# Performance work log

Hardware: AMD Instinct MI355X
Metric: run time of the kernel (lower is better)

The kernel has to match this reference:

```python
import jax, jax.numpy as jnp
import numpy as np

B, IN, P, H, OUT = 131072, 40, 128, 256, 1

def setup_inputs() -> dict:
    key = jax.random.key(0)
    ks = jax.random.split(key, 10)
    s_in, s_h = 1.0 / np.sqrt(IN), 1.0 / np.sqrt(H)
    return {
        "x_step": jax.random.normal(ks[0], (B, 1, IN), jnp.float32),
        "hidden_in": jax.random.normal(ks[1], (1, B, H), jnp.float32),
        "W_proj": jax.random.uniform(ks[2], (P, IN), jnp.float32, -s_in, s_in),
        "b_proj": jax.random.uniform(ks[3], (P,), jnp.float32, -s_in, s_in),
        "W_ih": jax.random.uniform(ks[4], (3 * H, P), jnp.float32, -s_h, s_h),
        "W_hh": jax.random.uniform(ks[5], (3 * H, H), jnp.float32, -s_h, s_h),
        "b_ih": jax.random.uniform(ks[6], (3 * H,), jnp.float32, -s_h, s_h),
        "b_hh": jax.random.uniform(ks[7], (3 * H,), jnp.float32, -s_h, s_h),
        "W_head": jax.random.uniform(ks[8], (OUT, H), jnp.float32, -s_h, s_h),
        "b_head": jax.random.uniform(ks[9], (OUT,), jnp.float32, -s_h, s_h),
    }

def reference(x_step, hidden_in, W_proj, b_proj, W_ih, W_hh, b_ih, b_hh, W_head, b_head):
    # input projection: [B,1,IN] -> [B,P]
    x = jnp.einsum('bi,pi->bp', x_step[:, 0, :], W_proj) + b_proj
    h = hidden_in[0]  # [B,H]
    # single GRU step (PyTorch gate layout: reset, update, new)
    gi = jnp.einsum('bp,gp->bg', x, W_ih) + b_ih  # [B,3H]
    gh = jnp.einsum('bh,gh->bg', h, W_hh) + b_hh  # [B,3H]
    i_r, i_z, i_n = jnp.split(gi, 3, axis=-1)
    h_r, h_z, h_n = jnp.split(gh, 3, axis=-1)
    r = jax.nn.sigmoid(i_r + h_r)
    z = jax.nn.sigmoid(i_z + h_z)
    n = jnp.tanh(i_n + r * h_n)
    h_new = (1.0 - z) * n + z * h  # [B,H]
    pred = jnp.einsum('bh,oh->bo', h_new, W_head) + b_head  # [B,OUT]
    return pred[:, None, :], h_new[None]  # ([B,1,OUT], [1,B,H])
```

## Files before the change

kernel.cpp:

```cpp
#include <hip/hip_runtime.h>

#define B_N 131072
#define IN_N 40
#define H_N 256

typedef __bf16 bf16x8 __attribute__((ext_vector_type(8)));
typedef __bf16 bf16x4 __attribute__((ext_vector_type(4)));
typedef float f32x4 __attribute__((ext_vector_type(4)));

#define MFMA(a, b, c) __builtin_amdgcn_mfma_f32_16x16x32_bf16(a, b, c, 0, 0, 0)

#define WSF 0
#define WSH 49152
#define WSBI 245760
#define PREP_N (245760 + 768 + B_N)

__global__ void prep(const float* __restrict__ Wp, const float* __restrict__ bp,
                     const float* __restrict__ Wih, const float* __restrict__ Whh,
                     const float* __restrict__ bih, const float* __restrict__ bhead,
                     __bf16* __restrict__ wsb, float* __restrict__ out) {
  int i = blockIdx.x * 256 + threadIdx.x;
  if (i < WSH) {
    int g = i >> 6, kk = i & 63;
    float v = 0.f;
    if (kk < IN_N) {
      for (int p = 0; p < 128; ++p) v += Wih[g * 128 + p] * Wp[p * IN_N + kk];
    }
    wsb[i] = (__bf16)v;
  } else if (i < WSBI) {
    wsb[i] = (__bf16)Whh[i - WSH];
  } else if (i < WSBI + 768) {
    int g = i - WSBI;
    float v = bih[g];
    for (int p = 0; p < 128; ++p) v += Wih[g * 128 + p] * bp[p];
    ((float*)(wsb + WSBI))[g] = v;
  } else if (i < PREP_N) {
    out[i - (WSBI + 768)] = bhead[0];
  }
}

__global__ __launch_bounds__(512, 2) void gru_v6(
    const float* __restrict__ x, const float* __restrict__ h0,
    const __bf16* __restrict__ wsb, const float* __restrict__ bhh,
    const float* __restrict__ Whead, float* __restrict__ out) {
  __shared__ __bf16 hs[2][64][264];
  __shared__ __bf16 xs[2][64][72];

  const int tid = threadIdx.x;
  const int lane = tid & 63;
  const int w = tid >> 6;
  const int l15 = lane & 15;
  const int l4 = lane >> 4;
  const int koff = l4 * 8;

  const int b = blockIdx.x;
  const int v = (b & 7) * 64 + (b >> 3);
  const int half = v & 1;
  const int tile0 = (v >> 1) * 8;
  const int col = half * 128 + w * 16 + l15;

  const __bf16* WH = wsb + WSH;
  const __bf16* WF = wsb + WSF;
  bf16x8 whR[8], whZ[8], whN[8], wfR[2], wfZ[2], wfN[2];
#pragma unroll
  for (int ks = 0; ks < 8; ++ks) {
    const int k = ks * 32 + koff;
    whR[ks] = *reinterpret_cast<const bf16x8*>(WH + (size_t)col * 256 + k);
    whZ[ks] = *reinterpret_cast<const bf16x8*>(WH + (size_t)(256 + col) * 256 + k);
    whN[ks] = *reinterpret_cast<const bf16x8*>(WH + (size_t)(512 + col) * 256 + k);
  }
#pragma unroll
  for (int ks = 0; ks < 2; ++ks) {
    const int k = ks * 32 + koff;
    wfR[ks] = *reinterpret_cast<const bf16x8*>(WF + (size_t)col * 64 + k);
    wfZ[ks] = *reinterpret_cast<const bf16x8*>(WF + (size_t)(256 + col) * 64 + k);
    wfN[ks] = *reinterpret_cast<const bf16x8*>(WF + (size_t)(512 + col) * 64 + k);
  }
  const float* bfused = (const float*)(wsb + WSBI);
  const float bR = bfused[col] + bhh[col];
  const float bZ = bfused[256 + col] + bhh[256 + col];
  const float bI = bfused[512 + col];
  const float bH = bhh[512 + col];
  const float whead = Whead[col];

  auto stage = [&](int buf, int row0) {
    const float* hb = h0 + (size_t)row0 * H_N;
#pragma unroll
    for (int j = 0; j < 8; ++j) {
      const int flat = (tid + j * 512) * 4;
      const int r = flat >> 8, c = flat & 255;
      float4 vv = *reinterpret_cast<const float4*>(hb + flat);
      bf16x4 u;
      u[0] = (__bf16)vv.x; u[1] = (__bf16)vv.y; u[2] = (__bf16)vv.z; u[3] = (__bf16)vv.w;
      *reinterpret_cast<bf16x4*>(&hs[buf][r][c]) = u;
    }
    const float* xb = x + (size_t)row0 * IN_N;
#pragma unroll
    for (int j = 0; j < 5; ++j) {
      const int i = tid + j * 512;
      xs[buf][i / 40][i % 40] = (__bf16)xb[i];
    }
#pragma unroll
    for (int j = 0; j < 3; ++j) {
      const int i = tid + j * 512;
      xs[buf][i / 24][40 + i % 24] = (__bf16)0.f;
    }
  };

  stage(0, tile0 * 64);
  __syncthreads();

  for (int t = 0; t < 8; ++t) {
    const int cur = t & 1;
    const int row0 = (tile0 + t) * 64;
    if (t < 7) stage(cur ^ 1, row0 + 64);

    f32x4 aR[4], aZ[4], aI[4], aH[4];
#pragma unroll
    for (int mi = 0; mi < 4; ++mi) {
      aR[mi] = (f32x4){bR, bR, bR, bR};
      aZ[mi] = (f32x4){bZ, bZ, bZ, bZ};
      aI[mi] = (f32x4){bI, bI, bI, bI};
      aH[mi] = (f32x4){bH, bH, bH, bH};
    }
#pragma unroll
    for (int ks = 0; ks < 2; ++ks) {
#pragma unroll
      for (int mi = 0; mi < 4; ++mi) {
        const bf16x8 a = *reinterpret_cast<const bf16x8*>(&xs[cur][mi * 16 + l15][ks * 32 + koff]);
        aR[mi] = MFMA(a, wfR[ks], aR[mi]);
        aZ[mi] = MFMA(a, wfZ[ks], aZ[mi]);
        aI[mi] = MFMA(a, wfN[ks], aI[mi]);
      }
    }
#pragma unroll
    for (int ks = 0; ks < 8; ++ks) {
#pragma unroll
      for (int mi = 0; mi < 4; ++mi) {
        const bf16x8 a = *reinterpret_cast<const bf16x8*>(&hs[cur][mi * 16 + l15][ks * 32 + koff]);
        aR[mi] = MFMA(a, whR[ks], aR[mi]);
        aZ[mi] = MFMA(a, whZ[ks], aZ[mi]);
        aH[mi] = MFMA(a, whN[ks], aH[mi]);
      }
    }
    float ps[4][4];
#pragma unroll
    for (int mi = 0; mi < 4; ++mi) {
#pragma unroll
      for (int r = 0; r < 4; ++r) {
        const int row = mi * 16 + l4 * 4 + r;
        const float rg = 1.f / (1.f + __expf(-aR[mi][r]));
        const float zg = 1.f / (1.f + __expf(-aZ[mi][r]));
        const float e2 = __expf(2.f * (aI[mi][r] + rg * aH[mi][r]));
        const float ng = (e2 - 1.f) / (e2 + 1.f);
        const float hv = (float)hs[cur][row][col];
        const float hn = (1.f - zg) * ng + zg * hv;
        out[(size_t)B_N + (size_t)(row0 + row) * H_N + col] = hn;
        ps[mi][r] = hn * whead;
      }
    }
#pragma unroll
    for (int mi = 0; mi < 4; ++mi)
#pragma unroll
      for (int r = 0; r < 4; ++r) {
        float s = ps[mi][r];
        s += __shfl_xor(s, 1);
        s += __shfl_xor(s, 2);
        s += __shfl_xor(s, 4);
        s += __shfl_xor(s, 8);
        if (l15 == 0) atomicAdd(&out[row0 + mi * 16 + l4 * 4 + r], s);
      }
    __syncthreads();
  }
}

extern "C" void kernel_launch(void* const* d_in, const int* in_sizes, int n_in,
                              void* d_out, int out_size, void* d_ws, size_t ws_size,
                              hipStream_t stream) {
  const float* x     = (const float*)d_in[0];
  const float* h0    = (const float*)d_in[1];
  const float* Wp    = (const float*)d_in[2];
  const float* bp    = (const float*)d_in[3];
  const float* Wih   = (const float*)d_in[4];
  const float* Whh   = (const float*)d_in[5];
  const float* bih   = (const float*)d_in[6];
  const float* bhh   = (const float*)d_in[7];
  const float* Whead = (const float*)d_in[8];
  const float* bhead = (const float*)d_in[9];
  float* out = (float*)d_out;
  __bf16* wsb = (__bf16*)d_ws;

  prep<<<(PREP_N + 255) / 256, 256, 0, stream>>>(Wp, bp, Wih, Whh, bih, bhead, wsb, out);
  gru_v6<<<512, 512, 0, stream>>>(x, h0, wsb, bhh, Whead, out);
}
```

Measured before the change: 216.2 us.

## Stream weight K-slices through LDS with async global_load_lds and larger row tiles

Weights are no longer held in registers per wave. They are pre-permuted in prep into K-slice-major tiles and streamed into double-buffered LDS via global_load_lds, one slice per step with a barrier each. Each block now computes a 128-row by 128-column tile, with waves arranged 2x4, and register-staged h/x prefetch for the next tile. This frees registers and raises per-wave MFMA work, but adds 10 barriers per tile, drops occupancy to one block per CU, and re-reads h0 in fp32 from global memory for the update.

Measured after the change: 421.9 us. 95.2% more time.

```diff
diff --git a/kernel.cpp b/kernel.cpp
--- a/kernel.cpp
+++ b/kernel.cpp
@@ -6,12 +6,13 @@
 
 typedef __bf16 bf16x8 __attribute__((ext_vector_type(8)));
 typedef __bf16 bf16x4 __attribute__((ext_vector_type(4)));
+typedef __bf16 bf16x2 __attribute__((ext_vector_type(2)));
 typedef float f32x4 __attribute__((ext_vector_type(4)));
 
 #define MFMA(a, b, c) __builtin_amdgcn_mfma_f32_16x16x32_bf16(a, b, c, 0, 0, 0)
 
-#define WSF 0
-#define WSH 49152
+#define WSGH 0
+#define WSGI 196608
 #define WSBI 245760
 #define PREP_N (245760 + 768 + B_N)
 
@@ -20,15 +21,21 @@
                      const float* __restrict__ bih, const float* __restrict__ bhead,
                      __bf16* __restrict__ wsb, float* __restrict__ out) {
   int i = blockIdx.x * 256 + threadIdx.x;
-  if (i < WSH) {
-    int g = i >> 6, kk = i & 63;
+  if (i < WSGI) {
+    int e8 = i & 7, col = (i >> 3) & 127, q = (i >> 10) & 3,
+        hf = (i >> 12) & 1, ks = (i >> 13) & 7, g = i >> 16;
+    int gcol = hf * 128 + col, k = ks * 32 + q * 8 + e8;
+    wsb[i] = (__bf16)Whh[(g * 256 + gcol) * 256 + k];
+  } else if (i < WSBI) {
+    int j = i - WSGI;
+    int e8 = j & 7, col = (j >> 3) & 127, q = (j >> 10) & 3,
+        hf = (j >> 12) & 1, ks2 = (j >> 13) & 1, g = j >> 14;
+    int gcol = hf * 128 + col, k = ks2 * 32 + q * 8 + e8;
     float v = 0.f;
-    if (kk < IN_N) {
-      for (int p = 0; p < 128; ++p) v += Wih[g * 128 + p] * Wp[p * IN_N + kk];
-    }
+    if (k < IN_N)
+      for (int p = 0; p < 128; ++p)
+        v += Wih[(g * 256 + gcol) * 128 + p] * Wp[p * IN_N + k];
     wsb[i] = (__bf16)v;
-  } else if (i < WSBI) {
-    wsb[i] = (__bf16)Whh[i - WSH];
   } else if (i < WSBI + 768) {
     int g = i - WSBI;
     float v = bih[g];
@@ -39,12 +46,19 @@
   }
 }
 
-__global__ __launch_bounds__(512, 2) void gru_v6(
+__device__ __forceinline__ void gload16(const __bf16* g, __bf16* l) {
+  __builtin_amdgcn_global_load_lds(
+      (const __attribute__((address_space(1))) void*)g,
+      (__attribute__((address_space(3))) void*)l, 16, 0, 0);
+}
+
+__global__ __launch_bounds__(512, 1) void gru_v11(
     const float* __restrict__ x, const float* __restrict__ h0,
     const __bf16* __restrict__ wsb, const float* __restrict__ bhh,
     const float* __restrict__ Whead, float* __restrict__ out) {
-  __shared__ __bf16 hs[2][64][264];
-  __shared__ __bf16 xs[2][64][72];
+  __shared__ __bf16 hs[128][264];
+  __shared__ __bf16 xs[128][72];
+  __shared__ __bf16 Bb[2][12288];
 
   const int tid = threadIdx.x;
   const int lane = tid & 63;
@@ -52,124 +66,162 @@
   const int l15 = lane & 15;
   const int l4 = lane >> 4;
   const int koff = l4 * 8;
-
-  const int b = blockIdx.x;
-  const int v = (b & 7) * 64 + (b >> 3);
-  const int half = v & 1;
-  const int tile0 = (v >> 1) * 8;
-  const int col = half * 128 + w * 16 + l15;
-
-  const __bf16* WH = wsb + WSH;
-  const __bf16* WF = wsb + WSF;
-  bf16x8 whR[8], whZ[8], whN[8], wfR[2], wfZ[2], wfN[2];
-#pragma unroll
-  for (int ks = 0; ks < 8; ++ks) {
-    const int k = ks * 32 + koff;
-    whR[ks] = *reinterpret_cast<const bf16x8*>(WH + (size_t)col * 256 + k);
-    whZ[ks] = *reinterpret_cast<const bf16x8*>(WH + (size_t)(256 + col) * 256 + k);
-    whN[ks] = *reinterpret_cast<const bf16x8*>(WH + (size_t)(512 + col) * 256 + k);
+  const int rw = w >> 2, cw = w & 3;
+
+  const int hf = blockIdx.x >> 8;
+  const int rgrp = blockIdx.x & 255;
+  const size_t row0 = (size_t)rgrp * 512;
+
+  const int colL = cw * 32 + l15;
+  const int col0 = hf * 128 + colL;
+  const int bofs = l4 * 1024 + colL * 8;
+
+  const float* bfused = (const float*)(wsb + WSBI);
+  float bR[2], bZ[2], bI[2], bH[2], wh[2];
+#pragma unroll
+  for (int ni = 0; ni < 2; ++ni) {
+    const int c = col0 + ni * 16;
+    bR[ni] = bfused[c] + bhh[c];
+    bZ[ni] = bfused[256 + c] + bhh[256 + c];
+    bI[ni] = bfused[512 + c];
+    bH[ni] = bhh[512 + c];
+    wh[ni] = Whead[c];
   }
-#pragma unroll
-  for (int ks = 0; ks < 2; ++ks) {
-    const int k = ks * 32 + koff;
-    wfR[ks] = *reinterpret_cast<const bf16x8*>(WF + (size_t)col * 64 + k);
-    wfZ[ks] = *reinterpret_cast<const bf16x8*>(WF + (size_t)(256 + col) * 64 + k);
-    wfN[ks] = *reinterpret_cast<const bf16x8*>(WF + (size_t)(512 + col) * 64 + k);
-  }
-  const float* bfused = (const float*)(wsb + WSBI);
-  const float bR = bfused[col] + bhh[col];
-  const float bZ = bfused[256 + col] + bhh[256 + col];
-  const float bI = bfused[512 + col];
-  const float bH = bhh[512 + col];
-  const float whead = Whead[col];
-
-  auto stage = [&](int buf, int row0) {
-    const float* hb = h0 + (size_t)row0 * H_N;
-#pragma unroll
-    for (int j = 0; j < 8; ++j) {
-      const int flat = (tid + j * 512) * 4;
-      const int r = flat >> 8, c = flat & 255;
-      float4 vv = *reinterpret_cast<const float4*>(hb + flat);
+
+  for (int j = tid; j < 128 * 32; j += 512) xs[j >> 5][40 + (j & 31)] = (__bf16)0.f;
+
+  bf16x4 sh[16];
+  bf16x2 sx[5];
+  auto issueStage = [&](int t) {
+    const float* hb = h0 + (row0 + (size_t)t * 128) * H_N;
+#pragma unroll
+    for (int k = 0; k < 16; ++k) {
+      const float4 v = *reinterpret_cast<const float4*>(hb + (size_t)(tid + k * 512) * 4);
       bf16x4 u;
-      u[0] = (__bf16)vv.x; u[1] = (__bf16)vv.y; u[2] = (__bf16)vv.z; u[3] = (__bf16)vv.w;
-      *reinterpret_cast<bf16x4*>(&hs[buf][r][c]) = u;
-    }
-    const float* xb = x + (size_t)row0 * IN_N;
-#pragma unroll
-    for (int j = 0; j < 5; ++j) {
-      const int i = tid + j * 512;
-      xs[buf][i / 40][i % 40] = (__bf16)xb[i];
-    }
-#pragma unroll
-    for (int j = 0; j < 3; ++j) {
-      const int i = tid + j * 512;
-      xs[buf][i / 24][40 + i % 24] = (__bf16)0.f;
-    }
-  };
-
-  stage(0, tile0 * 64);
+      u[0] = (__bf16)v.x; u[1] = (__bf16)v.y; u[2] = (__bf16)v.z; u[3] = (__bf16)v.w;
+      sh[k] = u;
+    }
+    const float* xb = x + (row0 + (size_t)t * 128) * IN_N;
+#pragma unroll
+    for (int k = 0; k < 5; ++k) {
+      const float2 v = *reinterpret_cast<const float2*>(xb + (size_t)(tid + k * 512) * 2);
+      bf16x2 u;
+      u[0] = (__bf16)v.x; u[1] = (__bf16)v.y;
+      sx[k] = u;
+    }
+  };
+  auto writeStage = [&]() {
+#pragma unroll
+    for (int k = 0; k < 16; ++k) {
+      const int f = tid + k * 512;
+      *reinterpret_cast<bf16x4*>(&hs[f >> 6][(f & 63) * 4]) = sh[k];
+    }
+#pragma unroll
+    for (int k = 0; k < 5; ++k) {
+      const int f = tid + k * 512;
+      *reinterpret_cast<bf16x2*>(&xs[f / 20][(f % 20) * 2]) = sx[k];
+    }
+  };
+
+  auto issueB = [&](int sn) {
+    const int buf = sn & 1;
+#pragma unroll
+    for (int g = 0; g < 3; ++g) {
+      const __bf16* gp = (sn < 2)
+          ? wsb + WSGI + (size_t)((g * 2 + sn) * 2 + hf) * 4096 + w * 512 + lane * 8
+          : wsb + WSGH + (size_t)((g * 8 + (sn - 2)) * 2 + hf) * 4096 + w * 512 + lane * 8;
+      gload16(gp, &Bb[buf][g * 4096 + w * 512]);
+    }
+  };
+
+  f32x4 aR[4][2], aZ[4][2], aI[4][2], aH[4][2];
+  auto step = [&](int s) {
+    const int buf = s & 1;
+    bf16x8 b[3][2];
+#pragma unroll
+    for (int g = 0; g < 3; ++g)
+#pragma unroll
+      for (int ni = 0; ni < 2; ++ni)
+        b[g][ni] = *reinterpret_cast<const bf16x8*>(&Bb[buf][g * 4096 + bofs + ni * 128]);
+#pragma unroll
+    for (int mi = 0; mi < 4; ++mi) {
+      const int row = rw * 64 + mi * 16 + l15;
+      const bf16x8 a = (s < 2)
+          ? *reinterpret_cast<const bf16x8*>(&xs[row][s * 32 + koff])
+          : *reinterpret_cast<const bf16x8*>(&hs[row][(s - 2) * 32 + koff]);
+#pragma unroll
+      for (int ni = 0; ni < 2; ++ni) {
+        aR[mi][ni] = MFMA(a, b[0][ni], aR[mi][ni]);
+        aZ[mi][ni] = MFMA(a, b[1][ni], aZ[mi][ni]);
+        if (s < 2) aI[mi][ni] = MFMA(a, b[2][ni], aI[mi][ni]);
+        else       aH[mi][ni] = MFMA(a, b[2][ni], aH[mi][ni]);
+      }
+    }
+    __syncthreads();
+  };
+
+  issueStage(0);
+  writeStage();
+  issueB(0);
   __syncthreads();
 
-  for (int t = 0; t < 8; ++t) {
-    const int cur = t & 1;
-    const int row0 = (tile0 + t) * 64;
-    if (t < 7) stage(cur ^ 1, row0 + 64);
-
-    f32x4 aR[4], aZ[4], aI[4], aH[4];
+  for (int t = 0; t < 4; ++t) {
+#pragma unroll
+    for (int mi = 0; mi < 4; ++mi)
+#pragma unroll
+      for (int ni = 0; ni < 2; ++ni) {
+        aR[mi][ni] = (f32x4){bR[ni], bR[ni], bR[ni], bR[ni]};
+        aZ[mi][ni] = (f32x4){bZ[ni], bZ[ni], bZ[ni], bZ[ni]};
+        aI[mi][ni] = (f32x4){bI[ni], bI[ni], bI[ni], bI[ni]};
+        aH[mi][ni] = (f32x4){bH[ni], bH[ni], bH[ni], bH[ni]};
+      }
+
+#pragma unroll
+    for (int s = 0; s < 10; ++s) {
+      issueB(s == 9 ? 0 : s + 1);
+      if (s == 2 && t < 3) issueStage(t + 1);
+      step(s);
+    }
+
+    const size_t trow = row0 + (size_t)t * 128;
+    float ps[4][4];
+#pragma unroll
+    for (int mi = 0; mi < 4; ++mi)
+#pragma unroll
+      for (int r = 0; r < 4; ++r) ps[mi][r] = 0.f;
 #pragma unroll
     for (int mi = 0; mi < 4; ++mi) {
-      aR[mi] = (f32x4){bR, bR, bR, bR};
-      aZ[mi] = (f32x4){bZ, bZ, bZ, bZ};
-      aI[mi] = (f32x4){bI, bI, bI, bI};
-      aH[mi] = (f32x4){bH, bH, bH, bH};
-    }
-#pragma unroll
-    for (int ks = 0; ks < 2; ++ks) {
-#pragma unroll
-      for (int mi = 0; mi < 4; ++mi) {
-        const bf16x8 a = *reinterpret_cast<const bf16x8*>(&xs[cur][mi * 16 + l15][ks * 32 + koff]);
-        aR[mi] = MFMA(a, wfR[ks], aR[mi]);
-        aZ[mi] = MFMA(a, wfZ[ks], aZ[mi]);
-        aI[mi] = MFMA(a, wfN[ks], aI[mi]);
-      }
-    }
-#pragma unroll
-    for (int ks = 0; ks < 8; ++ks) {
-#pragma unroll
-      for (int mi = 0; mi < 4; ++mi) {
-        const bf16x8 a = *reinterpret_cast<const bf16x8*>(&hs[cur][mi * 16 + l15][ks * 32 + koff]);
-        aR[mi] = MFMA(a, whR[ks], aR[mi]);
-        aZ[mi] = MFMA(a, whZ[ks], aZ[mi]);
-        aH[mi] = MFMA(a, whN[ks], aH[mi]);
-      }
-    }
-    float ps[4][4];
-#pragma unroll
-    for (int mi = 0; mi < 4; ++mi) {
+      const int rloc = rw * 64 + mi * 16 + l4 * 4;
+#pragma unroll
+      for (int ni = 0; ni < 2; ++ni) {
+        const int c = col0 + ni * 16;
+#pragma unroll
+        for (int r = 0; r < 4; ++r) {
+          const float rg_ = 1.f / (1.f + __expf(-aR[mi][ni][r]));
+          const float zg = 1.f / (1.f + __expf(-aZ[mi][ni][r]));
+          const float e2 = __expf(2.f * (aI[mi][ni][r] + rg_ * aH[mi][ni][r]));
+          const float ng = (e2 - 1.f) / (e2 + 1.f);
+          const float hv = h0[(trow + rloc + r) * H_N + c];
+          const float hn = (1.f - zg) * ng + zg * hv;
+          out[(size_t)B_N + (trow + rloc + r) * H_N + c] = hn;
+          ps[mi][r] += hn * wh[ni];
+        }
+      }
+    }
+#pragma unroll
+    for (int mi = 0; mi < 4; ++mi)
 #pragma unroll
       for (int r = 0; r < 4; ++r) {
-        const int row = mi * 16 + l4 * 4 + r;
-        const float rg = 1.f / (1.f + __expf(-aR[mi][r]));
-        const float zg = 1.f / (1.f + __expf(-aZ[mi][r]));
-        const float e2 = __expf(2.f * (aI[mi][r] + rg * aH[mi][r]));
-        const float ng = (e2 - 1.f) / (e2 + 1.f);
-        const float hv = (float)hs[cur][row][col];
-        const float hn = (1.f - zg) * ng + zg * hv;
-        out[(size_t)B_N + (size_t)(row0 + row) * H_N + col] = hn;
-        ps[mi][r] = hn * whead;
-      }
-    }
-#pragma unroll
-    for (int mi = 0; mi < 4; ++mi)
-#pragma unroll
-      for (int r = 0; r < 4; ++r) {
-        float s = ps[mi][r];
-        s += __shfl_xor(s, 1);
-        s += __shfl_xor(s, 2);
-        s += __shfl_xor(s, 4);
-        s += __shfl_xor(s, 8);
-        if (l15 == 0) atomicAdd(&out[row0 + mi * 16 + l4 * 4 + r], s);
-      }
+        float s2 = ps[mi][r];
+        s2 += __shfl_xor(s2, 1);
+        s2 += __shfl_xor(s2, 2);
+        s2 += __shfl_xor(s2, 4);
+        s2 += __shfl_xor(s2, 8);
+        if (l15 == 0)
+          atomicAdd(&out[trow + rw * 64 + mi * 16 + l4 * 4 + r], s2);
+      }
+
+    if (t < 3) writeStage();
     __syncthreads();
   }
 }
@@ -191,5 +243,5 @@
   __bf16* wsb = (__bf16*)d_ws;
 
   prep<<<(PREP_N + 255) / 256, 256, 0, stream>>>(Wp, bp, Wih, Whh, bih, bhead, wsb, out);
-  gru_v6<<<512, 512, 0, stream>>>(x, h0, wsb, bhh, Whead, out);
-}
+  gru_v11<<<512, 512, 0, stream>>>(x, h0, wsb, bhh, Whead, out);
+}
```
